# Performance work log

Hardware: AMD Instinct MI355X
Metric: run time of the kernel (lower is better)

## Reference

```python
import jax, jax.numpy as jnp
import numpy as np


def setup_inputs() -> dict:
    key = jax.random.key(0)
    k1, k2 = jax.random.split(key)
    B, L, D = 8, 2048, 256
    x = jax.random.normal(k1, (B, L, D), dtype=jnp.float32)
    x_mask = jax.random.randint(k2, (B, L), 0, 2).astype(bool)  # True = padded key position
    return {"x": x, "x_mask": x_mask}


def reference(x, x_mask):
    # x: [B, L, D], x_mask: [B, L] bool (True = masked/padding)
    B, L, D = x.shape
    # Unscaled self-attention scores: [B, L, L]
    scores = jnp.einsum('bld,bmd->blm', x, x)
    # Diagonal exclusion: score of token with itself set to 0 (not -inf!)
    eye = jnp.eye(L, dtype=bool)
    scores = jnp.where(eye[None, :, :], jnp.float32(0.0), scores)
    # Padding mask: mask key columns with -inf (applied after diagonal zeroing,
    # so a masked diagonal entry ends up -inf, matching the torch order of ops)
    scores = jnp.where(x_mask[:, None, :], -jnp.inf, scores)
    a = jax.nn.softmax(scores, axis=2)
    return jnp.einsum('blm,bmd->bld', a, x)
```

## Files before the change

kernel.cpp:

```cpp
#include <hip/hip_runtime.h>
#include <hip/hip_bf16.h>

#define B_ 8
#define L_ 2048
#define D_ 256
#define BK 32
#define KSPLIT 2
#define KQ (L_/KSPLIT)
#define NIT (KQ/BK)
#define PSTR 40
#define NROW (B_*L_)
#define NE ((size_t)B_*L_*D_)
#define THR 6.0f
#define MINIT (-1e30f)

typedef __attribute__((ext_vector_type(8))) _Float16 f16x8;
typedef __attribute__((ext_vector_type(4))) _Float16 hf4;
typedef __attribute__((ext_vector_type(4))) float f32x4;

#define MFMA16F(a,b,c) __builtin_amdgcn_mfma_f32_16x16x32_f16((a),(b),(c),0,0,0)
#define NEG_INF (-__builtin_inff())
#define GLL(src,dst) __builtin_amdgcn_global_load_lds( \
    (const __attribute__((address_space(1))) void*)(src), \
    (__attribute__((address_space(3))) void*)(dst), 16, 0, 0)

__device__ __forceinline__ f32x4 fmax4(f32x4 a, f32x4 b){
  f32x4 r;
  r[0]=fmaxf(a[0],b[0]); r[1]=fmaxf(a[1],b[1]);
  r[2]=fmaxf(a[2],b[2]); r[3]=fmaxf(a[3],b[3]);
  return r;
}

__global__ void prep_k(const float* __restrict__ x,
                       _Float16* __restrict__ x16,
                       _Float16* __restrict__ vtl){
  __shared__ _Float16 T[64][258];
  const int t = threadIdx.x;
  const int l0 = blockIdx.x*64, b = blockIdx.y;
  const int r = t>>5, c = (t&31)*8;
  #pragma unroll
  for (int p=0;p<8;++p){
    int row = r + p*8;
    size_t idx = ((size_t)(b*L_ + l0 + row))*D_ + c;
    float4 v0 = *(const float4*)(x + idx);
    float4 v1 = *(const float4*)(x + idx + 4);
    f16x8 h;
    h[0]=(_Float16)v0.x; h[1]=(_Float16)v0.y; h[2]=(_Float16)v0.z; h[3]=(_Float16)v0.w;
    h[4]=(_Float16)v1.x; h[5]=(_Float16)v1.y; h[6]=(_Float16)v1.z; h[7]=(_Float16)v1.w;
    *(f16x8*)(x16 + idx) = h;
    #pragma unroll
    for (int j=0;j<8;++j) T[row][c+j] = h[j];
  }
  __syncthreads();
  _Float16* vb = vtl + ((size_t)(b*64 + blockIdx.x*2))*8192;
  #pragma unroll
  for (int i=0;i<8;++i){
    int n = t + 256*i;
    int q = n & 1023, tile = n>>10;
    int d = q>>2, ph = q&3;
    int kc = ph ^ ((d>>1)&3);
    int k0 = tile*32 + kc*8;
    f16x8 h;
    #pragma unroll
    for (int j=0;j<8;++j) h[j] = T[k0+j][d];
    *(f16x8*)(vb + (size_t)n*8) = h;
  }
}

__launch_bounds__(256, 2)
__global__ void flash_k(const _Float16* __restrict__ x16,
                        const _Float16* __restrict__ vtl,
                        const int* __restrict__ mask,
                        _Float16* __restrict__ oall,
                        float* __restrict__ mll,
                        float* __restrict__ mm){
  __shared__ __attribute__((aligned(16))) _Float16 sK[2][8192];
  __shared__ __attribute__((aligned(16))) _Float16 sV[2][8192];
  __shared__ __attribute__((aligned(16))) _Float16 sP[2][4][16*PSTR];

  const int tid  = threadIdx.x;
  const int wave = tid >> 6, lane = tid & 63;
  const int quad = lane >> 4, l16 = lane & 15;
  const int b = blockIdx.y, z = blockIdx.z;
  const int q0w = blockIdx.x*64 + wave*16;
  const int sw = l16 & 7, vsw = (l16>>1)&3;

  f16x8 qh[8];
  {
    const _Float16* qr = x16 + ((size_t)(b*L_ + q0w + l16))*D_;
    #pragma unroll
    for (int ks=0; ks<8; ++ks)
      qh[ks] = *(const f16x8*)(qr + ks*32 + quad*8);
  }
  unsigned long long mb = 0;
  {
    const int* mrow = mask + b*L_ + z*KQ;
    #pragma unroll
    for (int j=0;j<64;++j)
      mb |= (unsigned long long)(mrow[j*16 + l16] ? 1u : 0u) << j;
  }

  f32x4 M = (f32x4){MINIT, MINIT, MINIT, MINIT};

  unsigned kof[4], vof[4], dof[4];
  #pragma unroll
  for (int i=0;i<4;++i){
    int c = (wave + i*4)*64 + lane;
    int r = c>>5, pk = c&31;
    kof[i] = (unsigned)(r*512 + ((pk ^ (r&7))*16));
    vof[i] = (unsigned)(c*16);
    dof[i] = (unsigned)((wave + i*4)*1024);
  }
  const char* kbase = (const char*)x16 + ((size_t)b*L_ + (size_t)z*KQ)*(D_*2);
  const char* vbase = (const char*)vtl + ((size_t)(b*64 + z*32))*16384;

  #pragma unroll
  for (int i=0;i<4;++i) GLL(kbase + kof[i], (char*)sK[0] + dof[i]);

  f32x4 O[16], Osum;
  #pragma unroll
  for (int i=0;i<16;i++) O[i] = (f32x4){0.f,0.f,0.f,0.f};
  Osum = (f32x4){0.f,0.f,0.f,0.f};
  f16x8 ones;
  #pragma unroll
  for (int j=0;j<8;++j) ones[j] = (_Float16)1.0f;

  __syncthreads();

  for (int it=0; it<NIT; ++it){
    if (it+1 < NIT){
      const char* kb2 = kbase + (size_t)(it+1)*16384;
      char* kd = (char*)sK[(it+1)&1];
      #pragma unroll
      for (int i=0;i<4;++i) GLL(kb2 + kof[i], kd + dof[i]);
    }
    {
      const char* vb2 = vbase + (size_t)it*16384;
      char* vd = (char*)sV[it&1];
      #pragma unroll
      for (int i=0;i<4;++i) GLL(vb2 + vof[i], vd + dof[i]);
    }
    const _Float16* kb = sK[it&1];

    f32x4 S[2];
    S[0]=(f32x4){0,0,0,0}; S[1]=(f32x4){0,0,0,0};
    #pragma unroll
    for (int ks=0; ks<8; ++ks){
      f16x8 b0 = *(const f16x8*)(kb + (     l16)*256 + (((ks*4+quad)^sw)*8));
      f16x8 b1 = *(const f16x8*)(kb + (16 + l16)*256 + (((ks*4+quad)^sw)*8));
      S[0] = MFMA16F(qh[ks], b0, S[0]);
      S[1] = MFMA16F(qh[ks], b1, S[1]);
    }

    if (it > 0){
      const _Float16* vb = sV[(it-1)&1];
      f16x8 pf = *(const f16x8*)(&sP[(it-1)&1][wave][l16*PSTR + quad*8]);
      #pragma unroll
      for (int vt=0; vt<16; ++vt){
        f16x8 bv = *(const f16x8*)(vb + (vt*16+l16)*32 + ((quad^vsw)*8));
        O[vt] = MFMA16F(pf, bv, O[vt]);
      }
      Osum = MFMA16F(pf, ones, Osum);
    }

    {
      const int d0 = q0w - (z*KQ + it*BK);
      if ((unsigned)d0 < 32u){
        const int ntd = d0 >> 4;
        #pragma unroll
        for (int r=0;r<4;++r)
          S[ntd][r] = (l16 == quad*4+r) ? 0.0f : S[ntd][r];
      }
    }
    {
      const unsigned mw = (unsigned)(mb >> (unsigned)(it*2));
      const float mk0 = (mw & 1u) ? NEG_INF : 0.0f;
      const float mk1 = (mw & 2u) ? NEG_INF : 0.0f;
      #pragma unroll
      for (int r=0;r<4;++r){ S[0][r] += mk0; S[1][r] += mk1; }
    }

    {
      f32x4 t = fmax4(S[0], S[1]);
      int ok = 1;
      #pragma unroll
      for (int r=0;r<4;++r) ok &= (t[r] <= M[r] + THR);
      if (!__all(ok)){
        #pragma unroll
        for (int off=1; off<16; off<<=1){
          f32x4 o;
          o[0]=__shfl_xor(t[0],off); o[1]=__shfl_xor(t[1],off);
          o[2]=__shfl_xor(t[2],off); o[3]=__shfl_xor(t[3],off);
          t = fmax4(t,o);
        }
        f32x4 mn = fmax4(M, t);
        float sc[4];
        #pragma unroll
        for (int r=0;r<4;++r) sc[r] = __expf(M[r] - mn[r]);
        #pragma unroll
        for (int vt=0; vt<16; ++vt){
          #pragma unroll
          for (int r=0;r<4;++r) O[vt][r] *= sc[r];
        }
        #pragma unroll
        for (int r=0;r<4;++r) Osum[r] *= sc[r];
        M = mn;
      }
    }

    #pragma unroll
    for (int r=0;r<4;++r){
      const int row = quad*4 + r;
      sP[it&1][wave][row*PSTR +      l16] = (_Float16)__expf(S[0][r] - M[r]);
      sP[it&1][wave][row*PSTR + 16 + l16] = (_Float16)__expf(S[1][r] - M[r]);
    }

    __syncthreads();
  }

  {
    const _Float16* vb = sV[(NIT-1)&1];
    f16x8 pf = *(const f16x8*)(&sP[(NIT-1)&1][wave][l16*PSTR + quad*8]);
    #pragma unroll
    for (int vt=0; vt<16; ++vt){
      f16x8 bv = *(const f16x8*)(vb + (vt*16+l16)*32 + ((quad^vsw)*8));
      O[vt] = MFMA16F(pf, bv, O[vt]);
    }
    Osum = MFMA16F(pf, ones, Osum);
  }

  {
    const int u = b*(L_/16) + blockIdx.x*4 + wave;
    _Float16* ob = oall + (size_t)z*NE + (size_t)u*4096;
    #pragma unroll
    for (int vt=0; vt<16; ++vt){
      hf4 hh;
      #pragma unroll
      for (int r=0;r<4;++r) hh[r] = (_Float16)O[vt][r];
      *(hf4*)(ob + vt*256 + lane*4) = hh;
    }
    if (l16 == 0){
      const int row = u*16 + quad*4;
      #pragma unroll
      for (int r=0;r<4;++r){
        mll[z*NROW + row + r] = Osum[r];
        mm [z*NROW + row + r] = M[r];
      }
    }
  }
}

__global__ void combine_k(float* __restrict__ out,
                          const _Float16* __restrict__ oall,
                          const float* __restrict__ mll,
                          const float* __restrict__ mm){
  __shared__ float T2[16][260];
  const int t = threadIdx.x, u = blockIdx.x;
  const int quad = (t>>4)&3, l16 = t&15;
  const int row0 = u*16 + quad*4;

  f32x4 mz[KSPLIT], lz[KSPLIT];
  #pragma unroll
  for (int zc=0; zc<KSPLIT; ++zc){
    mz[zc] = *(const f32x4*)(mm  + zc*NROW + row0);
    lz[zc] = *(const f32x4*)(mll + zc*NROW + row0);
  }
  f32x4 ms = mz[0];
  #pragma unroll
  for (int zc=1; zc<KSPLIT; ++zc) ms = fmax4(ms, mz[zc]);

  float sc[KSPLIT][4];
  f32x4 den = (f32x4){0.f,0.f,0.f,0.f};
  #pragma unroll
  for (int zc=0; zc<KSPLIT; ++zc){
    #pragma unroll
    for (int r=0;r<4;++r){
      sc[zc][r] = __expf(mz[zc][r] - ms[r]);
      den[r] += sc[zc][r] * lz[zc][r];
    }
  }
  float inv[4];
  #pragma unroll
  for (int r=0;r<4;++r) inv[r] = 1.0f/den[r];

  #pragma unroll
  for (int i=0;i<4;++i){
    const int f = t + 256*i;
    const int vt = f>>6;
    float acc[4] = {0.f,0.f,0.f,0.f};
    #pragma unroll
    for (int zc=0; zc<KSPLIT; ++zc){
      hf4 v = *(const hf4*)(oall + (size_t)zc*NE + (size_t)u*4096 + (size_t)f*4);
      #pragma unroll
      for (int r=0;r<4;++r) acc[r] += sc[zc][r] * (float)v[r];
    }
    #pragma unroll
    for (int r=0;r<4;++r) T2[quad*4+r][vt*16+l16] = acc[r]*inv[r];
  }
  __syncthreads();
  #pragma unroll
  for (int p=0;p<4;++p){
    const int row = (t>>6) + p*4, col = (t&63)*4;
    float4 vv = *(const float4*)&T2[row][col];
    *(float4*)(out + ((size_t)u*16 + row)*D_ + col) = vv;
  }
}

extern "C" void kernel_launch(void* const* d_in, const int* in_sizes, int n_in,
                              void* d_out, int out_size, void* d_ws, size_t ws_size,
                              hipStream_t stream) {
  const float* x    = (const float*)d_in[0];
  const int*   mask = (const int*)d_in[1];
  float*       out  = (float*)d_out;

  _Float16* x16  = (_Float16*)d_ws;
  _Float16* vtl  = x16 + NE;
  _Float16* oall = vtl + NE;
  float*    mll  = (float*)(oall + (size_t)KSPLIT*NE);
  float*    mm   = mll + (size_t)KSPLIT*NROW;

  prep_k   <<<dim3(L_/64, B_), dim3(256), 0, stream>>>(x, x16, vtl);
  flash_k  <<<dim3(L_/64, B_, KSPLIT), dim3(256), 0, stream>>>(x16, vtl, mask, oall, mll, mm);
  combine_k<<<dim3(NROW/16), dim3(256), 0, stream>>>(out, oall, mll, mm);
}
```

Baseline: 145.7 us.

## Fuse split-K combine into flash kernel via atomic ticket last-block reduction

Removes the separate combine kernel launch. Each flash block now increments a per-tile ticket after writing its partial results, and the last of the two split blocks merges both partials and writes the final fp32 output, reusing the K shared buffer as staging. Tickets are reset in the prep kernel. The change also raises the THR constant from 6 to 9, which likely governs a lazy rescale threshold in the online softmax, meaning fewer rescales at some risk to fp16 range and accuracy.

```diff
diff --git a/kernel.cpp b/kernel.cpp
--- a/kernel.cpp
+++ b/kernel.cpp
@@ -11,7 +11,7 @@
 #define PSTR 40
 #define NROW (B_*L_)
 #define NE ((size_t)B_*L_*D_)
-#define THR 6.0f
+#define THR 9.0f
 #define MINIT (-1e30f)
 
 typedef __attribute__((ext_vector_type(8))) _Float16 f16x8;
@@ -33,10 +33,12 @@
 
 __global__ void prep_k(const float* __restrict__ x,
                        _Float16* __restrict__ x16,
-                       _Float16* __restrict__ vtl){
+                       _Float16* __restrict__ vtl,
+                       int* __restrict__ ticket){
   __shared__ _Float16 T[64][258];
   const int t = threadIdx.x;
   const int l0 = blockIdx.x*64, b = blockIdx.y;
+  if (t == 0) ticket[b*(L_/64) + blockIdx.x] = 0;
   const int r = t>>5, c = (t&31)*8;
   #pragma unroll
   for (int p=0;p<8;++p){
@@ -73,10 +75,13 @@
                         const int* __restrict__ mask,
                         _Float16* __restrict__ oall,
                         float* __restrict__ mll,
-                        float* __restrict__ mm){
+                        float* __restrict__ mm,
+                        float* __restrict__ out,
+                        int* __restrict__ ticket){
   __shared__ __attribute__((aligned(16))) _Float16 sK[2][8192];
   __shared__ __attribute__((aligned(16))) _Float16 sV[2][8192];
   __shared__ __attribute__((aligned(16))) _Float16 sP[2][4][16*PSTR];
+  __shared__ int who;
 
   const int tid  = threadIdx.x;
   const int wave = tid >> 6, lane = tid & 63;
@@ -248,61 +253,54 @@
       }
     }
   }
-}
-
-__global__ void combine_k(float* __restrict__ out,
-                          const _Float16* __restrict__ oall,
-                          const float* __restrict__ mll,
-                          const float* __restrict__ mm){
-  __shared__ float T2[16][260];
-  const int t = threadIdx.x, u = blockIdx.x;
-  const int quad = (t>>4)&3, l16 = t&15;
-  const int row0 = u*16 + quad*4;
-
-  f32x4 mz[KSPLIT], lz[KSPLIT];
-  #pragma unroll
-  for (int zc=0; zc<KSPLIT; ++zc){
-    mz[zc] = *(const f32x4*)(mm  + zc*NROW + row0);
-    lz[zc] = *(const f32x4*)(mll + zc*NROW + row0);
-  }
-  f32x4 ms = mz[0];
-  #pragma unroll
-  for (int zc=1; zc<KSPLIT; ++zc) ms = fmax4(ms, mz[zc]);
-
-  float sc[KSPLIT][4];
-  f32x4 den = (f32x4){0.f,0.f,0.f,0.f};
-  #pragma unroll
-  for (int zc=0; zc<KSPLIT; ++zc){
-    #pragma unroll
-    for (int r=0;r<4;++r){
-      sc[zc][r] = __expf(mz[zc][r] - ms[r]);
-      den[r] += sc[zc][r] * lz[zc][r];
-    }
-  }
-  float inv[4];
-  #pragma unroll
-  for (int r=0;r<4;++r) inv[r] = 1.0f/den[r];
-
-  #pragma unroll
-  for (int i=0;i<4;++i){
-    const int f = t + 256*i;
-    const int vt = f>>6;
-    float acc[4] = {0.f,0.f,0.f,0.f};
-    #pragma unroll
-    for (int zc=0; zc<KSPLIT; ++zc){
-      hf4 v = *(const hf4*)(oall + (size_t)zc*NE + (size_t)u*4096 + (size_t)f*4);
-      #pragma unroll
-      for (int r=0;r<4;++r) acc[r] += sc[zc][r] * (float)v[r];
-    }
-    #pragma unroll
-    for (int r=0;r<4;++r) T2[quad*4+r][vt*16+l16] = acc[r]*inv[r];
-  }
+
+  __threadfence();
+  if (tid == 0) who = atomicAdd(&ticket[b*(L_/64) + blockIdx.x], 1);
   __syncthreads();
-  #pragma unroll
-  for (int p=0;p<4;++p){
-    const int row = (t>>6) + p*4, col = (t&63)*4;
-    float4 vv = *(const float4*)&T2[row][col];
-    *(float4*)(out + ((size_t)u*16 + row)*D_ + col) = vv;
+  if (who != KSPLIT-1) return;
+  __threadfence();
+
+  {
+    float (*T2)[260] = reinterpret_cast<float(*)[260]>(&sK[0][0]);
+    const int quad2 = (tid>>4)&3, l162 = tid&15;
+    #pragma unroll 1
+    for (int g=0; g<4; ++g){
+      const int u = b*(L_/16) + blockIdx.x*4 + g;
+      const int row0 = u*16 + quad2*4;
+
+      f32x4 mz0 = *(const f32x4*)(mm  + row0);
+      f32x4 mz1 = *(const f32x4*)(mm  + NROW + row0);
+      f32x4 lz0 = *(const f32x4*)(mll + row0);
+      f32x4 lz1 = *(const f32x4*)(mll + NROW + row0);
+      f32x4 ms = fmax4(mz0, mz1);
+      float s0[4], s1[4], inv[4];
+      #pragma unroll
+      for (int r=0;r<4;++r){
+        s0[r] = __expf(mz0[r] - ms[r]);
+        s1[r] = __expf(mz1[r] - ms[r]);
+        inv[r] = 1.0f/(s0[r]*lz0[r] + s1[r]*lz1[r]);
+      }
+
+      #pragma unroll
+      for (int i=0;i<4;++i){
+        const int f = tid + 256*i;
+        const int vt = f>>6;
+        hf4 v0 = *(const hf4*)(oall + (size_t)u*4096 + (size_t)f*4);
+        hf4 v1 = *(const hf4*)(oall + NE + (size_t)u*4096 + (size_t)f*4);
+        #pragma unroll
+        for (int r=0;r<4;++r)
+          T2[quad2*4+r][vt*16+l162] =
+            (s0[r]*(float)v0[r] + s1[r]*(float)v1[r]) * inv[r];
+      }
+      __syncthreads();
+      #pragma unroll
+      for (int p=0;p<4;++p){
+        const int row = (tid>>6) + p*4, col = (tid&63)*4;
+        float4 vv = *(const float4*)&T2[row][col];
+        *(float4*)(out + ((size_t)u*16 + row)*D_ + col) = vv;
+      }
+      __syncthreads();
+    }
   }
 }
 
@@ -318,8 +316,9 @@
   _Float16* oall = vtl + NE;
   float*    mll  = (float*)(oall + (size_t)KSPLIT*NE);
   float*    mm   = mll + (size_t)KSPLIT*NROW;
-
-  prep_k   <<<dim3(L_/64, B_), dim3(256), 0, stream>>>(x, x16, vtl);
-  flash_k  <<<dim3(L_/64, B_, KSPLIT), dim3(256), 0, stream>>>(x16, vtl, mask, oall, mll, mm);
-  combine_k<<<dim3(NROW/16), dim3(256), 0, stream>>>(out, oall, mll, mm);
+  int*      tick = (int*)(mm + (size_t)KSPLIT*NROW);
+
+  prep_k <<<dim3(L_/64, B_), dim3(256), 0, stream>>>(x, x16, vtl, tick);
+  flash_k<<<dim3(L_/64, B_, KSPLIT), dim3(256), 0, stream>>>(
+      x16, vtl, mask, oall, mll, mm, out, tick);
 }
```

New measurement: 224.3 us. +54.0%, slower.
